# Performance work log

Measured on AMD Instinct MI355X. Metric: run time of the kernel, lower is better.

The kernel has to match this reference:

```python
import jax, jax.numpy as jnp
import numpy as np
import math

D_MODEL = 1024
NUM_HEADS = 16
D_K = D_MODEL // NUM_HEADS
B, T = 2, 2048


def setup_inputs() -> dict:
    key = jax.random.key(0)
    ks = jax.random.split(key, 9)
    s = 1.0 / math.sqrt(D_MODEL)
    inp = {
        'x': jax.random.normal(ks[0], (B, T, D_MODEL), dtype=jnp.float32),
        'mask': jnp.tril(jnp.ones((1, 1, T, T), dtype=jnp.int32)),
        'Wq': jax.random.uniform(ks[1], (D_MODEL, D_MODEL), jnp.float32, -s, s),
        'bq': jax.random.uniform(ks[2], (D_MODEL,), jnp.float32, -s, s),
        'Wk': jax.random.uniform(ks[3], (D_MODEL, D_MODEL), jnp.float32, -s, s),
        'bk': jax.random.uniform(ks[4], (D_MODEL,), jnp.float32, -s, s),
        'Wv': jax.random.uniform(ks[5], (D_MODEL, D_MODEL), jnp.float32, -s, s),
        'bv': jax.random.uniform(ks[6], (D_MODEL,), jnp.float32, -s, s),
        'Wo': jax.random.uniform(ks[7], (D_MODEL, D_MODEL), jnp.float32, -s, s),
        'bo': jax.random.uniform(ks[8], (D_MODEL,), jnp.float32, -s, s),
    }
    return inp


def reference(x, mask, Wq, bq, Wk, bk, Wv, bv, Wo, bo):
    Bsz, Tlen, C = x.shape
    # projections; torch Linear computes x @ W.T + b, here W stored as (in,out)-like square so use x @ W + b with W meaning W.T
    q = (x @ Wq + bq).reshape(Bsz, Tlen, NUM_HEADS, D_K).transpose(0, 2, 1, 3)
    k = (x @ Wk + bk).reshape(Bsz, Tlen, NUM_HEADS, D_K).transpose(0, 2, 1, 3)
    v = (x @ Wv + bv).reshape(Bsz, Tlen, NUM_HEADS, D_K).transpose(0, 2, 1, 3)
    scores = jnp.einsum('bhqd,bhkd->bhqk', q, k) / math.sqrt(D_K)  # (B,H,T,T)
    scores = jnp.where(mask == 0, -jnp.inf, scores)
    attn = jax.nn.softmax(scores, axis=-1)
    out = jnp.einsum('bhqk,bhkd->bhqd', attn, v)
    out = out.transpose(0, 2, 1, 3).reshape(Bsz, Tlen, C)
    return out @ Wo + bo
```

## Files before the change

kernel.cpp:

```cpp
#include <hip/hip_runtime.h>
#include <math.h>

typedef unsigned short ushort_t;
typedef short short8 __attribute__((ext_vector_type(8)));
typedef float f32x4 __attribute__((ext_vector_type(4)));

#define DMODEL 1024
#define NHEADS 16
#define DKH    64
#define BATCH  2
#define SEQ    2048
#define BT     (BATCH * SEQ)

__device__ __forceinline__ ushort_t f2bf(float f) {
    union { float f; unsigned u; } a; a.f = f;
    return (ushort_t)((a.u + 0x7FFFu + ((a.u >> 16) & 1u)) >> 16);
}

__device__ __forceinline__ void async_copy16(const ushort_t* g, ushort_t* l) {
    __builtin_amdgcn_global_load_lds(
        (__attribute__((address_space(1))) void*)g,
        (__attribute__((address_space(3))) void*)l, 16, 0, 0);
}

__global__ __launch_bounds__(256) void cast_x_kernel(
    const float* __restrict__ x, ushort_t* __restrict__ xb)
{
    size_t i = ((size_t)blockIdx.x * 256 + threadIdx.x) * 8;
    float4 a = *(const float4*)(x + i);
    float4 b = *(const float4*)(x + i + 4);
    union { ushort_t u[8]; short8 v; } r;
    r.u[0] = f2bf(a.x); r.u[1] = f2bf(a.y); r.u[2] = f2bf(a.z); r.u[3] = f2bf(a.w);
    r.u[4] = f2bf(b.x); r.u[5] = f2bf(b.y); r.u[6] = f2bf(b.z); r.u[7] = f2bf(b.w);
    *(short8*)(xb + i) = r.v;
}

__global__ __launch_bounds__(256) void wtrans_kernel(
    const float* __restrict__ Wq, const float* __restrict__ Wk,
    const float* __restrict__ Wv, const float* __restrict__ Wo,
    ushort_t* __restrict__ WqT, ushort_t* __restrict__ WkT,
    ushort_t* __restrict__ WvT, ushort_t* __restrict__ WoT)
{
    const int z = blockIdx.z;
    const float* W = (z == 0) ? Wq : (z == 1) ? Wk : (z == 2) ? Wv : Wo;
    ushort_t*   WT = (z == 0) ? WqT : (z == 1) ? WkT : (z == 2) ? WvT : WoT;

    __shared__ ushort_t tile[64][72];
    const int k0 = blockIdx.x * 64, n0 = blockIdx.y * 64;
    const int tid = threadIdx.x;

    const int r  = tid >> 2;
    const int cb = (tid & 3) * 16;
#pragma unroll
    for (int u = 0; u < 4; ++u) {
        float4 v = *(const float4*)(W + (size_t)(k0 + r) * DMODEL + n0 + cb + u * 4);
        union { ushort_t u4[4]; unsigned long long ll; } p;
        p.u4[0] = f2bf(v.x); p.u4[1] = f2bf(v.y); p.u4[2] = f2bf(v.z); p.u4[3] = f2bf(v.w);
        *(unsigned long long*)&tile[r][cb + u * 4] = p.ll;
    }
    __syncthreads();
    const int n  = tid >> 2;
    const int kb = (tid & 3) * 16;
#pragma unroll
    for (int half = 0; half < 2; ++half) {
        union { ushort_t u8[8]; short8 v; } p;
#pragma unroll
        for (int j = 0; j < 8; ++j) p.u8[j] = tile[kb + half * 8 + j][n];
        *(short8*)(WT + (size_t)(n0 + n) * DMODEL + k0 + kb + half * 8) = p.v;
    }
}

__device__ __forceinline__ void gemm_dbuf_128(
    const ushort_t* __restrict__ A, const ushort_t* __restrict__ B,
    int m0, int n0, ushort_t* At, ushort_t* Bt, f32x4 (&acc)[4][4])
{
    const int tid  = threadIdx.x;
    const int w    = tid >> 6, lane = tid & 63;
    const int l15  = lane & 15, quad = lane >> 4;
    const int wm   = w >> 1, wn = w & 1;
    const int srow = lane >> 3;
    const int scol = ((lane & 7) ^ srow) << 3;
    const int swz  = l15 & 7;

#pragma unroll
    for (int c = 0; c < 4; ++c) {
        int ch = w * 4 + c;
        async_copy16(A + (size_t)(m0 + ch * 8 + srow) * DMODEL + scol, At + ch * 512);
        async_copy16(B + (size_t)(n0 + ch * 8 + srow) * DMODEL + scol, Bt + ch * 512);
    }
    __syncthreads();

    for (int kt = 0; kt < DMODEL / 64; ++kt) {
        const int cur = (kt & 1) << 13;
        if (kt + 1 < DMODEL / 64) {
            const int nxt = cur ^ 8192;
            const int k0 = (kt + 1) * 64;
#pragma unroll
            for (int c = 0; c < 4; ++c) {
                int ch = w * 4 + c;
                async_copy16(A + (size_t)(m0 + ch * 8 + srow) * DMODEL + k0 + scol,
                             At + nxt + ch * 512);
                async_copy16(B + (size_t)(n0 + ch * 8 + srow) * DMODEL + k0 + scol,
                             Bt + nxt + ch * 512);
            }
        }
#pragma unroll
        for (int kk = 0; kk < 2; ++kk) {
            short8 af[4], bf[4];
#pragma unroll
            for (int t = 0; t < 4; ++t) {
                int ra = wm * 64 + t * 16 + l15;
                int rb = wn * 64 + t * 16 + l15;
                af[t] = *(const short8*)(At + cur + ra * 64 +
                                         (((kk * 4 + quad) ^ swz) << 3));
                bf[t] = *(const short8*)(Bt + cur + rb * 64 +
                                         (((kk * 4 + quad) ^ swz) << 3));
            }
#pragma unroll
            for (int mt = 0; mt < 4; ++mt)
#pragma unroll
                for (int nt = 0; nt < 4; ++nt)
                    acc[mt][nt] = __builtin_amdgcn_mfma_f32_16x16x32_bf16(
                        af[mt], bf[nt], acc[mt][nt], 0, 0, 0);
        }
        __syncthreads();
    }
}

__device__ __forceinline__ void gemm_dbuf_n64(
    const ushort_t* __restrict__ A, const ushort_t* __restrict__ B,
    int m0, int n0, ushort_t* At, ushort_t* Bt, f32x4 (&acc)[4][2])
{
    const int tid  = threadIdx.x;
    const int w    = tid >> 6, lane = tid & 63;
    const int l15  = lane & 15, quad = lane >> 4;
    const int wm   = w >> 1, wn = w & 1;
    const int srow = lane >> 3;
    const int scol = ((lane & 7) ^ srow) << 3;
    const int swz  = l15 & 7;

#pragma unroll
    for (int c = 0; c < 4; ++c) {
        int ch = w * 4 + c;
        async_copy16(A + (size_t)(m0 + ch * 8 + srow) * DMODEL + scol, At + ch * 512);
    }
#pragma unroll
    for (int c = 0; c < 2; ++c) {
        int ch = w * 2 + c;
        async_copy16(B + (size_t)(n0 + ch * 8 + srow) * DMODEL + scol, Bt + ch * 512);
    }
    __syncthreads();

    for (int kt = 0; kt < DMODEL / 64; ++kt) {
        const int curA = (kt & 1) << 13;
        const int curB = (kt & 1) << 12;
        if (kt + 1 < DMODEL / 64) {
            const int k0 = (kt + 1) * 64;
#pragma unroll
            for (int c = 0; c < 4; ++c) {
                int ch = w * 4 + c;
                async_copy16(A + (size_t)(m0 + ch * 8 + srow) * DMODEL + k0 + scol,
                             At + (curA ^ 8192) + ch * 512);
            }
#pragma unroll
            for (int c = 0; c < 2; ++c) {
                int ch = w * 2 + c;
                async_copy16(B + (size_t)(n0 + ch * 8 + srow) * DMODEL + k0 + scol,
                             Bt + (curB ^ 4096) + ch * 512);
            }
        }
#pragma unroll
        for (int kk = 0; kk < 2; ++kk) {
            short8 af[4], bf[2];
#pragma unroll
            for (int t = 0; t < 4; ++t) {
                int ra = wm * 64 + t * 16 + l15;
                af[t] = *(const short8*)(At + curA + ra * 64 +
                                         (((kk * 4 + quad) ^ swz) << 3));
            }
#pragma unroll
            for (int t = 0; t < 2; ++t) {
                int rb = wn * 32 + t * 16 + l15;
                bf[t] = *(const short8*)(Bt + curB + rb * 64 +
                                         (((kk * 4 + quad) ^ swz) << 3));
            }
#pragma unroll
            for (int mt = 0; mt < 4; ++mt)
#pragma unroll
                for (int nt = 0; nt < 2; ++nt)
                    acc[mt][nt] = __builtin_amdgcn_mfma_f32_16x16x32_bf16(
                        af[mt], bf[nt], acc[mt][nt], 0, 0, 0);
        }
        __syncthreads();
    }
}

__global__ __launch_bounds__(256) void qkv_gemm(
    const ushort_t* __restrict__ xb,
    const ushort_t* __restrict__ WqT, const ushort_t* __restrict__ WkT,
    const ushort_t* __restrict__ WvT,
    const float* __restrict__ bq, const float* __restrict__ bk,
    const float* __restrict__ bv,
    ushort_t* __restrict__ Qb, ushort_t* __restrict__ Kb, ushort_t* __restrict__ VTo)
{
    const int z = blockIdx.z;
    const ushort_t* WT = (z == 0) ? WqT : (z == 1) ? WkT : WvT;
    const float* bias  = (z == 0) ? bq : (z == 1) ? bk : bv;

    __shared__ ushort_t At[2 * 8192];
    __shared__ ushort_t Bt[2 * 8192];
    const int m0 = blockIdx.x * 128, n0 = blockIdx.y * 128;

    f32x4 zero = {0.f, 0.f, 0.f, 0.f};
    f32x4 acc[4][4];
#pragma unroll
    for (int i = 0; i < 4; ++i)
#pragma unroll
        for (int j = 0; j < 4; ++j) acc[i][j] = zero;

    gemm_dbuf_128(xb, WT, m0, n0, At, Bt, acc);

    const int tid = threadIdx.x, w = tid >> 6, lane = tid & 63;
    const int l15 = lane & 15, quad = lane >> 4;
    const int wm = w >> 1, wn = w & 1;

    float bcol[4];
#pragma unroll
    for (int nt = 0; nt < 4; ++nt) bcol[nt] = bias[n0 + wn * 64 + nt * 16 + l15];

    if (z == 2) {
#pragma unroll
        for (int mt = 0; mt < 4; ++mt) {
            int row0 = m0 + wm * 64 + mt * 16 + quad * 4;
            int b = row0 >> 11, t = row0 & (SEQ - 1);
            int tb = t & ~63;
            int idxp = ((mt & 1) << 2) | (quad << 3) | ((mt >> 1) << 5);
#pragma unroll
            for (int nt = 0; nt < 4; ++nt) {
                int col = n0 + wn * 64 + nt * 16 + l15;
                int h = col >> 6, d = col & 63;
                union { ushort_t u4[4]; unsigned long long ll; } pk;
#pragma unroll
                for (int reg = 0; reg < 4; ++reg)
                    pk.u4[reg] = f2bf(acc[mt][nt][reg] + bcol[nt]);
                *(unsigned long long*)(VTo +
                    ((size_t)(b * NHEADS + h) * DKH + d) * SEQ + tb + idxp) = pk.ll;
            }
        }
    } else {
        ushort_t* out = (z == 0) ? Qb : Kb;
#pragma unroll
        for (int mt = 0; mt < 4; ++mt)
#pragma unroll
            for (int reg = 0; reg < 4; ++reg) {
                int row = m0 + wm * 64 + mt * 16 + quad * 4 + reg;
                int b = row >> 11, t = row & (SEQ - 1);
#pragma unroll
                for (int nt = 0; nt < 4; ++nt) {
                    int col = n0 + wn * 64 + nt * 16 + l15;
                    int h = col >> 6, d = col & 63;
                    out[((((size_t)b * NHEADS + h) * SEQ + t) << 6) + d] =
                        f2bf(acc[mt][nt][reg] + bcol[nt]);
                }
            }
    }
}

__global__ __launch_bounds__(256) void attn_kernel(
    const ushort_t* __restrict__ Qb, const ushort_t* __restrict__ Kb,
    const ushort_t* __restrict__ VT, ushort_t* __restrict__ AO)
{
    const int bi = blockIdx.x;
    const int bh = bi & 31;
    const int b  = bh >> 4, h = bh & 15;
    const int qq = bi >> 5;
    const int tid = threadIdx.x, w = tid >> 6, lane = tid & 63;
    const int l15 = lane & 15, quad = lane >> 4;

    __shared__ ushort_t Kt[2][64 * 64];
    __shared__ ushort_t Vt[2][64 * 64];

    const ushort_t* Kbase = Kb + (((size_t)bh * SEQ) << 6);
    const ushort_t* Vbase = VT + (size_t)bh * DKH * SEQ;

    const int srow = lane >> 3;
    const int schx = (lane & 7) ^ srow;
    const int swz  = l15 & 7;
    const f32x4 zero = {0.f, 0.f, 0.f, 0.f};
    const float cexp = 0.18033688011112042f;

    for (int job = 0; job < 2; ++job) {
        const int qt = job ? (31 - qq) : qq;
        const int q0 = qt * 64;
        const int nk = qt + 1;

        short8 qa[2];
#pragma unroll
        for (int ks = 0; ks < 2; ++ks)
            qa[ks] = *(const short8*)(
                Qb + (((size_t)bh * SEQ + q0 + w * 16 + l15) << 6) + ks * 32 + quad * 8);

        float l_i = 0.f;
        f32x4 o[4];
#pragma unroll
        for (int dt = 0; dt < 4; ++dt) o[dt] = zero;

#pragma unroll
        for (int c = 0; c < 2; ++c) {
            int chunk = w * 2 + c;
            async_copy16(Kbase + (((size_t)(chunk * 8 + srow)) << 6) + schx * 8,
                         &Kt[0][chunk * 512]);
            async_copy16(Vbase + (size_t)(chunk * 8 + srow) * SEQ + schx * 8,
                         &Vt[0][chunk * 512]);
        }
        __syncthreads();

        for (int kt = 0; kt < nk; ++kt) {
            const int buf = kt & 1;
            if (kt + 1 < nk) {
                const int kt0n = (kt + 1) * 64;
#pragma unroll
                for (int c = 0; c < 2; ++c) {
                    int chunk = w * 2 + c;
                    async_copy16(Kbase + (((size_t)(kt0n + chunk * 8 + srow)) << 6) + schx * 8,
                                 &Kt[buf ^ 1][chunk * 512]);
                    async_copy16(Vbase + (size_t)(chunk * 8 + srow) * SEQ + kt0n + schx * 8,
                                 &Vt[buf ^ 1][chunk * 512]);
                }
            }

            short8 kf[4][2], vf[2][4];
#pragma unroll
            for (int kt_i = 0; kt_i < 4; ++kt_i)
#pragma unroll
                for (int ks = 0; ks < 2; ++ks)
                    kf[kt_i][ks] = *(const short8*)&Kt[buf][(kt_i * 16 + l15) * 64 +
                                                            (((ks * 4 + quad) ^ swz) << 3)];
#pragma unroll
            for (int g = 0; g < 2; ++g)
#pragma unroll
                for (int dt = 0; dt < 4; ++dt)
                    vf[g][dt] = *(const short8*)&Vt[buf][(dt * 16 + l15) * 64 +
                                                         ((((g << 2) | quad) ^ swz) << 3)];

            f32x4 sc[4];
#pragma unroll
            for (int kt_i = 0; kt_i < 4; ++kt_i) sc[kt_i] = zero;
#pragma unroll
            for (int ks = 0; ks < 2; ++ks)
#pragma unroll
                for (int kt_i = 0; kt_i < 4; ++kt_i)
                    sc[kt_i] = __builtin_amdgcn_mfma_f32_16x16x32_bf16(
                        kf[kt_i][ks], qa[ks], sc[kt_i], 0, 0, 0);

            const bool domask = (kt == qt);
            const int qabs = q0 + w * 16 + l15;
            unsigned pka[4], pkb[4];
            float lp = 0.f;
#pragma unroll
            for (int kt_i = 0; kt_i < 4; ++kt_i) {
                unsigned u[4];
#pragma unroll
                for (int r = 0; r < 4; ++r) {
                    float p = exp2f(cexp * sc[kt_i][r]);
                    if (domask && (kt * 64 + kt_i * 16 + quad * 4 + r) > qabs) p = 0.f;
                    u[r] = __float_as_uint(p) & 0xFFFF0000u;
                    lp += __uint_as_float(u[r]);
                }
                pka[kt_i] = (u[0] >> 16) | u[1];
                pkb[kt_i] = (u[2] >> 16) | u[3];
            }
            l_i += lp;

#pragma unroll
            for (int g = 0; g < 2; ++g) {
                union { unsigned u[4]; short8 v; } pf;
                pf.u[0] = pka[2 * g];
                pf.u[1] = pkb[2 * g];
                pf.u[2] = pka[2 * g + 1];
                pf.u[3] = pkb[2 * g + 1];
#pragma unroll
                for (int dt = 0; dt < 4; ++dt)
                    o[dt] = __builtin_amdgcn_mfma_f32_16x16x32_bf16(
                        pf.v, vf[g][dt], o[dt], 0, 0, 0);
            }

            __syncthreads();
        }

        float l = l_i;
        l += __shfl_xor(l, 16);
        l += __shfl_xor(l, 32);
        float inv = 1.0f / l;
#pragma unroll
        for (int r = 0; r < 4; ++r) {
            float invr = __shfl(inv, quad * 4 + r, 16);
            int t = q0 + w * 16 + quad * 4 + r;
#pragma unroll
            for (int dt = 0; dt < 4; ++dt)
                AO[((size_t)b * SEQ + t) * DMODEL + h * 64 + dt * 16 + l15] =
                    f2bf(o[dt][r] * invr);
        }
    }
}

__global__ __launch_bounds__(256) void out_gemm(
    const ushort_t* __restrict__ AO, const ushort_t* __restrict__ WoT,
    const float* __restrict__ bo, float* __restrict__ out)
{
    __shared__ ushort_t At[2 * 8192];
    __shared__ ushort_t Bt[2 * 4096];
    const int m0 = blockIdx.x * 128, n0 = blockIdx.y * 64;

    f32x4 zero = {0.f, 0.f, 0.f, 0.f};
    f32x4 acc[4][2];
#pragma unroll
    for (int i = 0; i < 4; ++i)
#pragma unroll
        for (int j = 0; j < 2; ++j) acc[i][j] = zero;

    gemm_dbuf_n64(AO, WoT, m0, n0, At, Bt, acc);

    const int tid = threadIdx.x, w = tid >> 6, lane = tid & 63;
    const int l15 = lane & 15, quad = lane >> 4;
    const int wm = w >> 1, wn = w & 1;

    float bcol[2];
#pragma unroll
    for (int nt = 0; nt < 2; ++nt) bcol[nt] = bo[n0 + wn * 32 + nt * 16 + l15];

#pragma unroll
    for (int mt = 0; mt < 4; ++mt)
#pragma unroll
        for (int reg = 0; reg < 4; ++reg) {
            int row = m0 + wm * 64 + mt * 16 + quad * 4 + reg;
#pragma unroll
            for (int nt = 0; nt < 2; ++nt) {
                int col = n0 + wn * 32 + nt * 16 + l15;
                out[(size_t)row * DMODEL + col] = acc[mt][nt][reg] + bcol[nt];
            }
        }
}

extern "C" void kernel_launch(void* const* d_in, const int* in_sizes, int n_in,
                              void* d_out, int out_size, void* d_ws, size_t ws_size,
                              hipStream_t stream)
{
    const float* x  = (const float*)d_in[0];
    const float* Wq = (const float*)d_in[2];
    const float* bq = (const float*)d_in[3];
    const float* Wk = (const float*)d_in[4];
    const float* bk = (const float*)d_in[5];
    const float* Wv = (const float*)d_in[6];
    const float* bv = (const float*)d_in[7];
    const float* Wo = (const float*)d_in[8];
    const float* bo = (const float*)d_in[9];
    float* out = (float*)d_out;

    ushort_t* ws = (ushort_t*)d_ws;
    size_t off = 0;
    ushort_t* xb  = ws + off; off += (size_t)BT * DMODEL;
    ushort_t* WqT = ws + off; off += (size_t)DMODEL * DMODEL;
    ushort_t* WkT = ws + off; off += (size_t)DMODEL * DMODEL;
    ushort_t* WvT = ws + off; off += (size_t)DMODEL * DMODEL;
    ushort_t* WoT = ws + off; off += (size_t)DMODEL * DMODEL;
    ushort_t* Qb  = ws + off; off += (size_t)BT * DMODEL;
    ushort_t* Kb  = ws + off; off += (size_t)BT * DMODEL;
    ushort_t* VTb = ws + off; off += (size_t)BT * DMODEL;
    ushort_t* AOb = ws + off; off += (size_t)BT * DMODEL;

    cast_x_kernel<<<(BT * DMODEL) / (256 * 8), 256, 0, stream>>>(x, xb);
    wtrans_kernel<<<dim3(16, 16, 4), 256, 0, stream>>>(
        Wq, Wk, Wv, Wo, WqT, WkT, WvT, WoT);
    qkv_gemm<<<dim3(BT / 128, DMODEL / 128, 3), 256, 0, stream>>>(
        xb, WqT, WkT, WvT, bq, bk, bv, Qb, Kb, VTb);
    attn_kernel<<<dim3(SEQ / 64 * NHEADS * BATCH / 2), 256, 0, stream>>>(
        Qb, Kb, VTb, AOb);
    out_gemm<<<dim3(BT / 128, DMODEL / 64), 256, 0, stream>>>(
        AOb, WoT, bo, out);
}
```

Before: 204.5 us.

## Merge prep kernels, compute softmax row sums via MFMA, reshape out-GEMM tile

Fuses the x cast and weight transpose kernels into one launch to save a kernel launch. In attention, the softmax denominator is now accumulated with an extra MFMA against a ones vector instead of scalar adds and cross-lane shuffles. Bf16 packing uses a byte permute, which truncates rather than rounds. The output GEMM tile changes from 128x64 to 64x128 with the warp layout swapped to match.

```diff
diff --git a/kernel.cpp b/kernel.cpp
--- a/kernel.cpp
+++ b/kernel.cpp
@@ -23,31 +23,34 @@
         (__attribute__((address_space(3))) void*)l, 16, 0, 0);
 }
 
-__global__ __launch_bounds__(256) void cast_x_kernel(
-    const float* __restrict__ x, ushort_t* __restrict__ xb)
-{
-    size_t i = ((size_t)blockIdx.x * 256 + threadIdx.x) * 8;
-    float4 a = *(const float4*)(x + i);
-    float4 b = *(const float4*)(x + i + 4);
-    union { ushort_t u[8]; short8 v; } r;
-    r.u[0] = f2bf(a.x); r.u[1] = f2bf(a.y); r.u[2] = f2bf(a.z); r.u[3] = f2bf(a.w);
-    r.u[4] = f2bf(b.x); r.u[5] = f2bf(b.y); r.u[6] = f2bf(b.z); r.u[7] = f2bf(b.w);
-    *(short8*)(xb + i) = r.v;
-}
-
-__global__ __launch_bounds__(256) void wtrans_kernel(
+__global__ __launch_bounds__(256) void prep_kernel(
+    const float* __restrict__ x, ushort_t* __restrict__ xb,
     const float* __restrict__ Wq, const float* __restrict__ Wk,
     const float* __restrict__ Wv, const float* __restrict__ Wo,
     ushort_t* __restrict__ WqT, ushort_t* __restrict__ WkT,
     ushort_t* __restrict__ WvT, ushort_t* __restrict__ WoT)
 {
-    const int z = blockIdx.z;
+    __shared__ ushort_t tile[64][72];
+    const int bx = blockIdx.x;
+    const int tid = threadIdx.x;
+
+    if (bx < 2048) {
+        size_t i = ((size_t)bx * 256 + tid) * 8;
+        float4 a = *(const float4*)(x + i);
+        float4 b = *(const float4*)(x + i + 4);
+        union { ushort_t u[8]; short8 v; } r;
+        r.u[0] = f2bf(a.x); r.u[1] = f2bf(a.y); r.u[2] = f2bf(a.z); r.u[3] = f2bf(a.w);
+        r.u[4] = f2bf(b.x); r.u[5] = f2bf(b.y); r.u[6] = f2bf(b.z); r.u[7] = f2bf(b.w);
+        *(short8*)(xb + i) = r.v;
+        return;
+    }
+
+    const int idx = bx - 2048;
+    const int z  = idx >> 8;
+    const int n0 = ((idx >> 4) & 15) * 64;
+    const int k0 = (idx & 15) * 64;
     const float* W = (z == 0) ? Wq : (z == 1) ? Wk : (z == 2) ? Wv : Wo;
     ushort_t*   WT = (z == 0) ? WqT : (z == 1) ? WkT : (z == 2) ? WvT : WoT;
-
-    __shared__ ushort_t tile[64][72];
-    const int k0 = blockIdx.x * 64, n0 = blockIdx.y * 64;
-    const int tid = threadIdx.x;
 
     const int r  = tid >> 2;
     const int cb = (tid & 3) * 16;
@@ -127,67 +130,67 @@
     }
 }
 
-__device__ __forceinline__ void gemm_dbuf_n64(
+__device__ __forceinline__ void gemm_dbuf_m64(
     const ushort_t* __restrict__ A, const ushort_t* __restrict__ B,
-    int m0, int n0, ushort_t* At, ushort_t* Bt, f32x4 (&acc)[4][2])
+    int m0, int n0, ushort_t* At, ushort_t* Bt, f32x4 (&acc)[2][4])
 {
     const int tid  = threadIdx.x;
     const int w    = tid >> 6, lane = tid & 63;
     const int l15  = lane & 15, quad = lane >> 4;
-    const int wm   = w >> 1, wn = w & 1;
+    const int wm   = w & 1, wn = w >> 1;
     const int srow = lane >> 3;
     const int scol = ((lane & 7) ^ srow) << 3;
     const int swz  = l15 & 7;
 
 #pragma unroll
+    for (int c = 0; c < 2; ++c) {
+        int ch = w * 2 + c;
+        async_copy16(A + (size_t)(m0 + ch * 8 + srow) * DMODEL + scol, At + ch * 512);
+    }
+#pragma unroll
     for (int c = 0; c < 4; ++c) {
         int ch = w * 4 + c;
-        async_copy16(A + (size_t)(m0 + ch * 8 + srow) * DMODEL + scol, At + ch * 512);
-    }
-#pragma unroll
-    for (int c = 0; c < 2; ++c) {
-        int ch = w * 2 + c;
         async_copy16(B + (size_t)(n0 + ch * 8 + srow) * DMODEL + scol, Bt + ch * 512);
     }
     __syncthreads();
 
     for (int kt = 0; kt < DMODEL / 64; ++kt) {
-        const int curA = (kt & 1) << 13;
-        const int curB = (kt & 1) << 12;
+        const int curA = (kt & 1) << 12;
+        const int curB = (kt & 1) << 13;
         if (kt + 1 < DMODEL / 64) {
             const int k0 = (kt + 1) * 64;
 #pragma unroll
+            for (int c = 0; c < 2; ++c) {
+                int ch = w * 2 + c;
+                async_copy16(A + (size_t)(m0 + ch * 8 + srow) * DMODEL + k0 + scol,
+                             At + (curA ^ 4096) + ch * 512);
+            }
+#pragma unroll
             for (int c = 0; c < 4; ++c) {
                 int ch = w * 4 + c;
-                async_copy16(A + (size_t)(m0 + ch * 8 + srow) * DMODEL + k0 + scol,
-                             At + (curA ^ 8192) + ch * 512);
-            }
-#pragma unroll
-            for (int c = 0; c < 2; ++c) {
-                int ch = w * 2 + c;
                 async_copy16(B + (size_t)(n0 + ch * 8 + srow) * DMODEL + k0 + scol,
-                             Bt + (curB ^ 4096) + ch * 512);
+                             Bt + (curB ^ 8192) + ch * 512);
             }
         }
 #pragma unroll
         for (int kk = 0; kk < 2; ++kk) {
-            short8 af[4], bf[2];
-#pragma unroll
-            for (int t = 0; t < 4; ++t) {
-                int ra = wm * 64 + t * 16 + l15;
+            short8 af[2], bf[4];
+#pragma unroll
+            for (int t = 0; t < 2; ++t) {
+                int ra = wm * 32 + t * 16 + l15;
                 af[t] = *(const short8*)(At + curA + ra * 64 +
                                          (((kk * 4 + quad) ^ swz) << 3));
             }
 #pragma unroll
-            for (int t = 0; t < 2; ++t) {
-                int rb = wn * 32 + t * 16 + l15;
+            for (int t = 0; t < 4; ++t) {
+                int rb = wn * 64 + t * 16 + l15;
                 bf[t] = *(const short8*)(Bt + curB + rb * 64 +
                                          (((kk * 4 + quad) ^ swz) << 3));
             }
 #pragma unroll
-            for (int mt = 0; mt < 4; ++mt)
-#pragma unroll
-                for (int nt = 0; nt < 2; ++nt)
+            for (int mt = 0; mt < 2; ++mt)
+#pragma unroll
+                for (int nt = 0; nt < 4; ++nt)
                     acc[mt][nt] = __builtin_amdgcn_mfma_f32_16x16x32_bf16(
                         af[mt], bf[nt], acc[mt][nt], 0, 0, 0);
         }
@@ -289,6 +292,10 @@
     const f32x4 zero = {0.f, 0.f, 0.f, 0.f};
     const float cexp = 0.18033688011112042f;
 
+    union { ushort_t u8[8]; short8 v; } ones;
+#pragma unroll
+    for (int j = 0; j < 8; ++j) ones.u8[j] = 0x3F80;
+
     for (int job = 0; job < 2; ++job) {
         const int qt = job ? (31 - qq) : qq;
         const int q0 = qt * 64;
@@ -300,7 +307,7 @@
             qa[ks] = *(const short8*)(
                 Qb + (((size_t)bh * SEQ + q0 + w * 16 + l15) << 6) + ks * 32 + quad * 8);
 
-        float l_i = 0.f;
+        f32x4 lacc = zero;
         f32x4 o[4];
 #pragma unroll
         for (int dt = 0; dt < 4; ++dt) o[dt] = zero;
@@ -356,21 +363,20 @@
             const bool domask = (kt == qt);
             const int qabs = q0 + w * 16 + l15;
             unsigned pka[4], pkb[4];
-            float lp = 0.f;
 #pragma unroll
             for (int kt_i = 0; kt_i < 4; ++kt_i) {
-                unsigned u[4];
+                float p[4];
 #pragma unroll
                 for (int r = 0; r < 4; ++r) {
-                    float p = exp2f(cexp * sc[kt_i][r]);
-                    if (domask && (kt * 64 + kt_i * 16 + quad * 4 + r) > qabs) p = 0.f;
-                    u[r] = __float_as_uint(p) & 0xFFFF0000u;
-                    lp += __uint_as_float(u[r]);
+                    float pv = exp2f(cexp * sc[kt_i][r]);
+                    if (domask && (kt * 64 + kt_i * 16 + quad * 4 + r) > qabs) pv = 0.f;
+                    p[r] = pv;
                 }
-                pka[kt_i] = (u[0] >> 16) | u[1];
-                pkb[kt_i] = (u[2] >> 16) | u[3];
-            }
-            l_i += lp;
+                pka[kt_i] = __builtin_amdgcn_perm(
+                    __float_as_uint(p[1]), __float_as_uint(p[0]), 0x07060302u);
+                pkb[kt_i] = __builtin_amdgcn_perm(
+                    __float_as_uint(p[3]), __float_as_uint(p[2]), 0x07060302u);
+            }
 
 #pragma unroll
             for (int g = 0; g < 2; ++g) {
@@ -379,6 +385,8 @@
                 pf.u[1] = pkb[2 * g];
                 pf.u[2] = pka[2 * g + 1];
                 pf.u[3] = pkb[2 * g + 1];
+                lacc = __builtin_amdgcn_mfma_f32_16x16x32_bf16(
+                    pf.v, ones.v, lacc, 0, 0, 0);
 #pragma unroll
                 for (int dt = 0; dt < 4; ++dt)
                     o[dt] = __builtin_amdgcn_mfma_f32_16x16x32_bf16(
@@ -388,18 +396,14 @@
             __syncthreads();
         }
 
-        float l = l_i;
-        l += __shfl_xor(l, 16);
-        l += __shfl_xor(l, 32);
-        float inv = 1.0f / l;
 #pragma unroll
         for (int r = 0; r < 4; ++r) {
-            float invr = __shfl(inv, quad * 4 + r, 16);
+            float inv = 1.0f / lacc[r];
             int t = q0 + w * 16 + quad * 4 + r;
 #pragma unroll
             for (int dt = 0; dt < 4; ++dt)
                 AO[((size_t)b * SEQ + t) * DMODEL + h * 64 + dt * 16 + l15] =
-                    f2bf(o[dt][r] * invr);
+                    f2bf(o[dt][r] * inv);
         }
     }
 }
@@ -408,35 +412,35 @@
     const ushort_t* __restrict__ AO, const ushort_t* __restrict__ WoT,
     const float* __restrict__ bo, float* __restrict__ out)
 {
-    __shared__ ushort_t At[2 * 8192];
-    __shared__ ushort_t Bt[2 * 4096];
-    const int m0 = blockIdx.x * 128, n0 = blockIdx.y * 64;
+    __shared__ ushort_t At[2 * 4096];
+    __shared__ ushort_t Bt[2 * 8192];
+    const int m0 = blockIdx.x * 64, n0 = blockIdx.y * 128;
 
     f32x4 zero = {0.f, 0.f, 0.f, 0.f};
-    f32x4 acc[4][2];
-#pragma unroll
-    for (int i = 0; i < 4; ++i)
-#pragma unroll
-        for (int j = 0; j < 2; ++j) acc[i][j] = zero;
-
-    gemm_dbuf_n64(AO, WoT, m0, n0, At, Bt, acc);
+    f32x4 acc[2][4];
+#pragma unroll
+    for (int i = 0; i < 2; ++i)
+#pragma unroll
+        for (int j = 0; j < 4; ++j) acc[i][j] = zero;
+
+    gemm_dbuf_m64(AO, WoT, m0, n0, At, Bt, acc);
 
     const int tid = threadIdx.x, w = tid >> 6, lane = tid & 63;
     const int l15 = lane & 15, quad = lane >> 4;
-    const int wm = w >> 1, wn = w & 1;
-
-    float bcol[2];
-#pragma unroll
-    for (int nt = 0; nt < 2; ++nt) bcol[nt] = bo[n0 + wn * 32 + nt * 16 + l15];
-
-#pragma unroll
-    for (int mt = 0; mt < 4; ++mt)
+    const int wm = w & 1, wn = w >> 1;
+
+    float bcol[4];
+#pragma unroll
+    for (int nt = 0; nt < 4; ++nt) bcol[nt] = bo[n0 + wn * 64 + nt * 16 + l15];
+
+#pragma unroll
+    for (int mt = 0; mt < 2; ++mt)
 #pragma unroll
         for (int reg = 0; reg < 4; ++reg) {
-            int row = m0 + wm * 64 + mt * 16 + quad * 4 + reg;
-#pragma unroll
-            for (int nt = 0; nt < 2; ++nt) {
-                int col = n0 + wn * 32 + nt * 16 + l15;
+            int row = m0 + wm * 32 + mt * 16 + quad * 4 + reg;
+#pragma unroll
+            for (int nt = 0; nt < 4; ++nt) {
+                int col = n0 + wn * 64 + nt * 16 + l15;
                 out[(size_t)row * DMODEL + col] = acc[mt][nt][reg] + bcol[nt];
             }
         }
@@ -469,13 +473,12 @@
     ushort_t* VTb = ws + off; off += (size_t)BT * DMODEL;
     ushort_t* AOb = ws + off; off += (size_t)BT * DMODEL;
 
-    cast_x_kernel<<<(BT * DMODEL) / (256 * 8), 256, 0, stream>>>(x, xb);
-    wtrans_kernel<<<dim3(16, 16, 4), 256, 0, stream>>>(
-        Wq, Wk, Wv, Wo, WqT, WkT, WvT, WoT);
+    prep_kernel<<<2048 + 1024, 256, 0, stream>>>(
+        x, xb, Wq, Wk, Wv, Wo, WqT, WkT, WvT, WoT);
     qkv_gemm<<<dim3(BT / 128, DMODEL / 128, 3), 256, 0, stream>>>(
         xb, WqT, WkT, WvT, bq, bk, bv, Qb, Kb, VTb);
     attn_kernel<<<dim3(SEQ / 64 * NHEADS * BATCH / 2), 256, 0, stream>>>(
         Qb, Kb, VTb, AOb);
-    out_gemm<<<dim3(BT / 128, DMODEL / 64), 256, 0, stream>>>(
+    out_gemm<<<dim3(BT / 64, DMODEL / 128), 256, 0, stream>>>(
         AOb, WoT, bo, out);
 }
```

Result: no change. 201.7 us (-1.3%).
